# Optimization experiments

Measured on AMD Instinct MI355X. Metric: run time of the kernel, lower is better.

## Reference

```python
import jax, jax.numpy as jnp
import numpy as np
from jax import lax

NUM_SAMPLE = 1024   # init_kwargs: num_sample
RADIUS = 0.1        # init_kwargs: ball_query_radius (compared against SQUARED distance, as in original)


def setup_inputs() -> dict:
    key = jax.random.key(0)
    x = jax.random.normal(key, (4, 32768, 131), dtype=jnp.float32)  # [B, N, 3+C]
    return {"x": x}


def _fps_single(pts, num_sample):
    # pts: [N, 3]. Faithful to source: seed index is overwritten at i=0, so the
    # only effect of the seed is the first distance update; we use a
    # deterministic seed of 0 instead of python random.randint.
    n = pts.shape[0]

    def step(carry, _):
        closest, sel = carry
        d = jnp.sum((pts[sel] - pts) ** 2, axis=-1)      # [N]
        closest = jnp.minimum(d, closest)
        sel = jnp.argmax(closest).astype(jnp.int32)
        return (closest, sel), sel

    init = (jnp.full((n,), jnp.inf, dtype=jnp.float32), jnp.int32(0))
    _, idx = lax.scan(step, init, None, length=num_sample)
    return idx  # [M] int32


def _ball_query_counts(pts, idx, radius):
    # pts: [N,3], idx: [M]. Original builds variable-length index lists; the
    # jit-static equivalent is the membership mask d2 <= radius. We return the
    # per-centroid member counts (summary of the mask).
    cent = pts[idx]                                                 # [M, 3]
    d2 = jnp.sum((cent[:, None, :] - pts[None, :, :]) ** 2, axis=-1)  # [M, N]
    return jnp.sum(d2 <= radius, axis=-1).astype(jnp.int32)          # [M]


def reference(x):
    pts = x[:, :, :3]                                    # [B, N, 3]
    idx = jax.vmap(lambda p: _fps_single(p, NUM_SAMPLE))(pts)            # [B, M]
    counts = jax.vmap(lambda p, i: _ball_query_counts(p, i, RADIUS))(pts, idx)  # [B, M]
    # Original forward returns x unchanged; idx/counts are returned as well so
    # the FPS + ball-query compute is observable and not dead-code-eliminated.
    return (x, idx, counts)
```

## Files before the change

### kernel.cpp

```cpp
#include <hip/hip_runtime.h>
#include <math.h>

#define B 4
#define N 32768
#define D 131
#define S 1024
#define RAD2 0.1f
#define G 16
#define TPB 256
#define PPT 8
#define NFPS (B * G)
#define COPY_BLOCKS 192

__global__ void pack_kernel(const float* __restrict__ x, float* __restrict__ ws) {
    int i = blockIdx.x * blockDim.x + threadIdx.x;
    if (i < B * N) {
        const float* __restrict__ s = x + (size_t)i * D;
        float a = s[0], bb = s[1], c = s[2];
        ws[i]             = a;
        ws[B * N + i]     = bb;
        ws[2 * B * N + i] = c;
        float4* w4 = (float4*)(ws + (size_t)3 * B * N);
        w4[i] = make_float4(a, bb, c, 0.0f);
    }
}

__launch_bounds__(TPB)
__global__ void fps_copy_kernel(const float* __restrict__ x,
                                const float* __restrict__ ws,
                                unsigned long long* __restrict__ gslot,
                                float* __restrict__ out_idx,
                                int* __restrict__ idx_int,
                                float* __restrict__ out_x) {
    if (blockIdx.x >= NFPS) {
        const size_t total4 = (size_t)B * N * D / 4;
        const float4* __restrict__ src = (const float4*)x;
        float4* __restrict__ dst = (float4*)out_x;
        for (size_t i = (size_t)(blockIdx.x - NFPS) * TPB + threadIdx.x; i < total4;
             i += (size_t)COPY_BLOCKS * TPB)
            dst[i] = src[i];
        return;
    }

    const int b = blockIdx.x >> 4;
    const int g = blockIdx.x & 15;
    const int t = threadIdx.x;
    const int lane = t & 63;
    const int w = t >> 6;

    __shared__ unsigned long long s_wk[2][4];
    __shared__ float s_bc[3];
    __shared__ unsigned s_tag;

    const float* __restrict__ px = ws + (size_t)b * N;
    const float* __restrict__ py = ws + (size_t)(B + b) * N;
    const float* __restrict__ pz = ws + (size_t)(2 * B + b) * N;
    const float4* __restrict__ p4 = (const float4*)(ws + (size_t)3 * B * N) + (size_t)b * N;
    unsigned long long* __restrict__ slots = gslot + (size_t)b * 2 * G;

    const int base = g * (N / G);
    float lx[PPT], ly[PPT], lz[PPT], lcl[PPT];
    #pragma unroll
    for (int i = 0; i < PPT / 2; ++i) {
        int p = base + 2 * t + 2 * TPB * i;
        float2 vx = *(const float2*)&px[p];
        float2 vy = *(const float2*)&py[p];
        float2 vz = *(const float2*)&pz[p];
        lx[2*i] = vx.x; lx[2*i+1] = vx.y;
        ly[2*i] = vy.x; ly[2*i+1] = vy.y;
        lz[2*i] = vz.x; lz[2*i+1] = vz.y;
        lcl[2*i] = INFINITY; lcl[2*i+1] = INFINITY;
    }
    if (t == 0) s_tag = 0;
    __syncthreads();

    float4 cq = p4[0];
    float cx = cq.x, cy = cq.y, cz = cq.z;

    for (int s = 0; s < S; ++s) {
        float best = -INFINITY;
        int   bidx = 0;
        #pragma unroll
        for (int i = 0; i < PPT / 2; ++i) {
            const int p = base + 2 * t + 2 * TPB * i;
            {
                float dx = __fsub_rn(cx, lx[2*i]);
                float dy = __fsub_rn(cy, ly[2*i]);
                float dz = __fsub_rn(cz, lz[2*i]);
                float d2 = __fadd_rn(__fadd_rn(__fmul_rn(dx, dx), __fmul_rn(dy, dy)),
                                     __fmul_rn(dz, dz));
                float c = fminf(lcl[2*i], d2);
                lcl[2*i] = c;
                if (c > best) { best = c; bidx = p; }
            }
            {
                float dx = __fsub_rn(cx, lx[2*i+1]);
                float dy = __fsub_rn(cy, ly[2*i+1]);
                float dz = __fsub_rn(cz, lz[2*i+1]);
                float d2 = __fadd_rn(__fadd_rn(__fmul_rn(dx, dx), __fmul_rn(dy, dy)),
                                     __fmul_rn(dz, dz));
                float c = fminf(lcl[2*i+1], d2);
                lcl[2*i+1] = c;
                if (c > best) { best = c; bidx = p + 1; }
            }
        }

        unsigned hi  = __float_as_uint(best);
        unsigned lo2 = (unsigned)(32767 - bidx);
        #define FPS_COMBINE(OHI, OLO) \
            { unsigned _oh = (OHI), _ol = (OLO); \
              if (_oh > hi || (_oh == hi && _ol > lo2)) { hi = _oh; lo2 = _ol; } }
        { unsigned a = (unsigned)__builtin_amdgcn_update_dpp(0, (int)hi, 0xB1, 0xf, 0xf, true);
          unsigned c2 = (unsigned)__builtin_amdgcn_update_dpp(0, (int)lo2, 0xB1, 0xf, 0xf, true);
          FPS_COMBINE(a, c2); }
        { unsigned a = (unsigned)__builtin_amdgcn_update_dpp(0, (int)hi, 0x4E, 0xf, 0xf, true);
          unsigned c2 = (unsigned)__builtin_amdgcn_update_dpp(0, (int)lo2, 0x4E, 0xf, 0xf, true);
          FPS_COMBINE(a, c2); }
        { unsigned a = (unsigned)__builtin_amdgcn_update_dpp(0, (int)hi, 0x141, 0xf, 0xf, true);
          unsigned c2 = (unsigned)__builtin_amdgcn_update_dpp(0, (int)lo2, 0x141, 0xf, 0xf, true);
          FPS_COMBINE(a, c2); }
        { unsigned a = (unsigned)__builtin_amdgcn_update_dpp(0, (int)hi, 0x140, 0xf, 0xf, true);
          unsigned c2 = (unsigned)__builtin_amdgcn_update_dpp(0, (int)lo2, 0x140, 0xf, 0xf, true);
          FPS_COMBINE(a, c2); }
        { unsigned a = (unsigned)__builtin_amdgcn_ds_swizzle((int)hi, 0x401F);
          unsigned c2 = (unsigned)__builtin_amdgcn_ds_swizzle((int)lo2, 0x401F);
          FPS_COMBINE(a, c2); }
        { unsigned a = (unsigned)__shfl_xor((int)hi, 32, 64);
          unsigned c2 = (unsigned)__shfl_xor((int)lo2, 32, 64);
          FPS_COMBINE(a, c2); }
        #undef FPS_COMBINE

        const int buf = s & 1;
        const unsigned tag = (unsigned)(s + 1);
        const unsigned long long mykey = ((unsigned long long)hi << 32) |
                                         ((unsigned long long)lo2 << 17) | tag;
        if (lane == 0) s_wk[buf][w] = mykey;
        __syncthreads();

        if (w == 0) {
            unsigned long long bk = s_wk[buf][0];
            #pragma unroll
            for (int j = 1; j < 4; ++j) { unsigned long long v = s_wk[buf][j]; if (v > bk) bk = v; }
            if (lane == 0)
                __hip_atomic_store(&slots[buf * G + g], bk, __ATOMIC_RELAXED,
                                   __HIP_MEMORY_SCOPE_AGENT);

            unsigned long long kk;
            unsigned long long* myslot = &slots[buf * G + (lane & 15)];
            do {
                kk = __hip_atomic_load(myslot, __ATOMIC_RELAXED, __HIP_MEMORY_SCOPE_AGENT);
            } while (__any((unsigned)(kk & 0x7FFull) != tag));

            const unsigned long long kko = kk;
            const int idxc = 32767 - (int)((kko >> 17) & 0x7FFF);
            const float4 cand = p4[idxc];

            #pragma unroll
            for (int off = 1; off < 16; off <<= 1) {
                unsigned long long o = (unsigned long long)__shfl_xor((long long)kk, off, 64);
                if (o > kk) kk = o;
            }
            unsigned long long mask = __ballot(kko == kk);
            int src = (int)(__ffsll((unsigned long long)mask) - 1);
            cx = __shfl(cand.x, src, 64);
            cy = __shfl(cand.y, src, 64);
            cz = __shfl(cand.z, src, 64);

            if (lane == 0) {
                s_bc[0] = cx; s_bc[1] = cy; s_bc[2] = cz;
                __threadfence_block();
                __hip_atomic_store(&s_tag, tag, __ATOMIC_RELAXED,
                                   __HIP_MEMORY_SCOPE_WORKGROUP);
                if (g == 0) {
                    int sel = 32767 - (int)((kk >> 17) & 0x7FFF);
                    out_idx[(size_t)b * S + s] = (float)sel;
                    idx_int[b * S + s] = sel;
                }
            }
        } else {
            while (__hip_atomic_load(&s_tag, __ATOMIC_RELAXED,
                                     __HIP_MEMORY_SCOPE_WORKGROUP) != tag) {}
            __threadfence_block();
            cx = s_bc[0]; cy = s_bc[1]; cz = s_bc[2];
        }
    }
}

__launch_bounds__(256)
__global__ void ballq_kernel(const float* __restrict__ ws,
                             const int* __restrict__ idx_int,
                             float* __restrict__ out_counts) {
    __shared__ int s_part[4];
    const int b = blockIdx.x >> 10;
    const int j = blockIdx.x & 1023;
    const int t = threadIdx.x;
    const float* __restrict__ px = ws + (size_t)b * N;
    const float* __restrict__ py = ws + (size_t)(B + b) * N;
    const float* __restrict__ pz = ws + (size_t)(2 * B + b) * N;

    const int ci = idx_int[b * S + j];
    const float cx = px[ci], cy = py[ci], cz = pz[ci];

    int cnt = 0;
    #pragma unroll 4
    for (int p = t; p < N; p += 256) {
        float dx = __fsub_rn(cx, px[p]);
        float dy = __fsub_rn(cy, py[p]);
        float dz = __fsub_rn(cz, pz[p]);
        float d2 = __fadd_rn(__fadd_rn(__fmul_rn(dx, dx), __fmul_rn(dy, dy)),
                             __fmul_rn(dz, dz));
        cnt += (d2 <= RAD2) ? 1 : 0;
    }
    #pragma unroll
    for (int off = 1; off < 64; off <<= 1)
        cnt += __shfl_xor(cnt, off, 64);
    if ((t & 63) == 0) s_part[t >> 6] = cnt;
    __syncthreads();
    if (t == 0)
        out_counts[b * S + j] = (float)(s_part[0] + s_part[1] + s_part[2] + s_part[3]);
}

extern "C" void kernel_launch(void* const* d_in, const int* in_sizes, int n_in,
                              void* d_out, int out_size, void* d_ws, size_t ws_size,
                              hipStream_t stream) {
    const float* x = (const float*)d_in[0];
    float* out = (float*)d_out;
    float* ws = (float*)d_ws;
    int* idx_int = (int*)(ws + (size_t)7 * B * N);
    unsigned long long* gslot = (unsigned long long*)(idx_int + B * S);

    float* out_x      = out;
    float* out_idx    = out + (size_t)B * N * D;
    float* out_counts = out_idx + (size_t)B * S;

    hipMemsetAsync(gslot, 0, (size_t)B * 2 * G * sizeof(unsigned long long), stream);

    hipLaunchKernelGGL(pack_kernel, dim3((B * N + 255) / 256), dim3(256), 0, stream, x, ws);
    hipLaunchKernelGGL(fps_copy_kernel, dim3(NFPS + COPY_BLOCKS), dim3(TPB), 0, stream,
                       x, ws, gslot, out_idx, idx_int, out_x);
    hipLaunchKernelGGL(ballq_kernel, dim3(B * S), dim3(256), 0, stream, ws, idx_int, out_counts);
}
```

Baseline: 1.938 ms.

## Halve FPS blocks per batch, stage points in LDS, pad and pipeline slot polling

Cuts the FPS blocks per batch from 16 to 8 and doubles threads per block to 512, which halves the number of blocks taking part in each cross-block argmax handshake. Point coordinates now live in shared memory instead of registers to relieve register pressure at the larger block size. Global sync slots are padded to separate cache lines, and polling keeps four outstanding loads with short sleeps to hide latency. The risks are the extra LDS reads on every FPS iteration and a larger intra-block reduction over 8 waves. The copy blocks also now run at 512 threads with the same stride constant.

```diff
diff --git a/kernel.cpp b/kernel.cpp
--- a/kernel.cpp
+++ b/kernel.cpp
@@ -6,11 +6,12 @@
 #define D 131
 #define S 1024
 #define RAD2 0.1f
-#define G 16
-#define TPB 256
+#define G 8
+#define TPB 512
 #define PPT 8
 #define NFPS (B * G)
 #define COPY_BLOCKS 192
+#define SLOT_STRIDE 8
 
 __global__ void pack_kernel(const float* __restrict__ x, float* __restrict__ ws) {
     int i = blockIdx.x * blockDim.x + threadIdx.x;
@@ -42,13 +43,14 @@
         return;
     }
 
-    const int b = blockIdx.x >> 4;
-    const int g = blockIdx.x & 15;
+    const int b = blockIdx.x >> 3;
+    const int g = blockIdx.x & 7;
     const int t = threadIdx.x;
     const int lane = t & 63;
     const int w = t >> 6;
 
-    __shared__ unsigned long long s_wk[2][4];
+    __shared__ float s_x[N / G], s_y[N / G], s_z[N / G];
+    __shared__ unsigned long long s_wk[2][8];
     __shared__ float s_bc[3];
     __shared__ unsigned s_tag;
 
@@ -56,19 +58,16 @@
     const float* __restrict__ py = ws + (size_t)(B + b) * N;
     const float* __restrict__ pz = ws + (size_t)(2 * B + b) * N;
     const float4* __restrict__ p4 = (const float4*)(ws + (size_t)3 * B * N) + (size_t)b * N;
-    unsigned long long* __restrict__ slots = gslot + (size_t)b * 2 * G;
+    unsigned long long* __restrict__ slots = gslot + (size_t)b * 2 * G * SLOT_STRIDE;
 
     const int base = g * (N / G);
-    float lx[PPT], ly[PPT], lz[PPT], lcl[PPT];
+    float lcl[PPT];
     #pragma unroll
     for (int i = 0; i < PPT / 2; ++i) {
-        int p = base + 2 * t + 2 * TPB * i;
-        float2 vx = *(const float2*)&px[p];
-        float2 vy = *(const float2*)&py[p];
-        float2 vz = *(const float2*)&pz[p];
-        lx[2*i] = vx.x; lx[2*i+1] = vx.y;
-        ly[2*i] = vy.x; ly[2*i+1] = vy.y;
-        lz[2*i] = vz.x; lz[2*i+1] = vz.y;
+        const int l = 2 * t + 2 * TPB * i;
+        *(float2*)&s_x[l] = *(const float2*)&px[base + l];
+        *(float2*)&s_y[l] = *(const float2*)&py[base + l];
+        *(float2*)&s_z[l] = *(const float2*)&pz[base + l];
         lcl[2*i] = INFINITY; lcl[2*i+1] = INFINITY;
     }
     if (t == 0) s_tag = 0;
@@ -82,26 +81,29 @@
         int   bidx = 0;
         #pragma unroll
         for (int i = 0; i < PPT / 2; ++i) {
-            const int p = base + 2 * t + 2 * TPB * i;
+            const int l = 2 * t + 2 * TPB * i;
+            float2 vx = *(const float2*)&s_x[l];
+            float2 vy = *(const float2*)&s_y[l];
+            float2 vz = *(const float2*)&s_z[l];
             {
-                float dx = __fsub_rn(cx, lx[2*i]);
-                float dy = __fsub_rn(cy, ly[2*i]);
-                float dz = __fsub_rn(cz, lz[2*i]);
+                float dx = __fsub_rn(cx, vx.x);
+                float dy = __fsub_rn(cy, vy.x);
+                float dz = __fsub_rn(cz, vz.x);
                 float d2 = __fadd_rn(__fadd_rn(__fmul_rn(dx, dx), __fmul_rn(dy, dy)),
                                      __fmul_rn(dz, dz));
                 float c = fminf(lcl[2*i], d2);
                 lcl[2*i] = c;
-                if (c > best) { best = c; bidx = p; }
+                if (c > best) { best = c; bidx = base + l; }
             }
             {
-                float dx = __fsub_rn(cx, lx[2*i+1]);
-                float dy = __fsub_rn(cy, ly[2*i+1]);
-                float dz = __fsub_rn(cz, lz[2*i+1]);
+                float dx = __fsub_rn(cx, vx.y);
+                float dy = __fsub_rn(cy, vy.y);
+                float dz = __fsub_rn(cz, vz.y);
                 float d2 = __fadd_rn(__fadd_rn(__fmul_rn(dx, dx), __fmul_rn(dy, dy)),
                                      __fmul_rn(dz, dz));
                 float c = fminf(lcl[2*i+1], d2);
                 lcl[2*i+1] = c;
-                if (c > best) { best = c; bidx = p + 1; }
+                if (c > best) { best = c; bidx = base + l + 1; }
             }
         }
 
@@ -140,23 +142,37 @@
         if (w == 0) {
             unsigned long long bk = s_wk[buf][0];
             #pragma unroll
-            for (int j = 1; j < 4; ++j) { unsigned long long v = s_wk[buf][j]; if (v > bk) bk = v; }
+            for (int j = 1; j < 8; ++j) { unsigned long long v = s_wk[buf][j]; if (v > bk) bk = v; }
             if (lane == 0)
-                __hip_atomic_store(&slots[buf * G + g], bk, __ATOMIC_RELAXED,
-                                   __HIP_MEMORY_SCOPE_AGENT);
-
-            unsigned long long kk;
-            unsigned long long* myslot = &slots[buf * G + (lane & 15)];
-            do {
-                kk = __hip_atomic_load(myslot, __ATOMIC_RELAXED, __HIP_MEMORY_SCOPE_AGENT);
-            } while (__any((unsigned)(kk & 0x7FFull) != tag));
-
-            const unsigned long long kko = kk;
+                __hip_atomic_store(&slots[((size_t)buf * G + g) * SLOT_STRIDE], bk,
+                                   __ATOMIC_RELAXED, __HIP_MEMORY_SCOPE_AGENT);
+
+            unsigned long long* myslot =
+                &slots[((size_t)buf * G + (lane & 7)) * SLOT_STRIDE];
+            #define POLL() __hip_atomic_load(myslot, __ATOMIC_RELAXED, __HIP_MEMORY_SCOPE_AGENT)
+            unsigned long long q0, q1, q2, q3, kko;
+            q0 = POLL(); __builtin_amdgcn_s_sleep(2);
+            q1 = POLL(); __builtin_amdgcn_s_sleep(2);
+            q2 = POLL(); __builtin_amdgcn_s_sleep(2);
+            q3 = POLL();
+            for (;;) {
+                if (!__any((unsigned)(q0 & 0x7FFull) != tag)) { kko = q0; break; }
+                q0 = POLL();
+                if (!__any((unsigned)(q1 & 0x7FFull) != tag)) { kko = q1; break; }
+                q1 = POLL();
+                if (!__any((unsigned)(q2 & 0x7FFull) != tag)) { kko = q2; break; }
+                q2 = POLL();
+                if (!__any((unsigned)(q3 & 0x7FFull) != tag)) { kko = q3; break; }
+                q3 = POLL();
+            }
+            #undef POLL
+
             const int idxc = 32767 - (int)((kko >> 17) & 0x7FFF);
             const float4 cand = p4[idxc];
 
+            unsigned long long kk = kko;
             #pragma unroll
-            for (int off = 1; off < 16; off <<= 1) {
+            for (int off = 1; off < 8; off <<= 1) {
                 unsigned long long o = (unsigned long long)__shfl_xor((long long)kk, off, 64);
                 if (o > kk) kk = o;
             }
@@ -233,7 +249,8 @@
     float* out_idx    = out + (size_t)B * N * D;
     float* out_counts = out_idx + (size_t)B * S;
 
-    hipMemsetAsync(gslot, 0, (size_t)B * 2 * G * sizeof(unsigned long long), stream);
+    hipMemsetAsync(gslot, 0,
+                   (size_t)B * 2 * G * SLOT_STRIDE * sizeof(unsigned long long), stream);
 
     hipLaunchKernelGGL(pack_kernel, dim3((B * N + 255) / 256), dim3(256), 0, stream, x, ws);
     hipLaunchKernelGGL(fps_copy_kernel, dim3(NFPS + COPY_BLOCKS), dim3(TPB), 0, stream,
```

New measurement: 2.298 ms. +18.6%, slower.
